# Performance work log

Hardware: AMD Instinct MI355X
Metric: run time of the kernel (lower is better)

The kernel has to match this reference:

```python
import jax, jax.numpy as jnp
import numpy as np

B, L, H = 2, 2048, 1024
NH, DK, DV = 4, 256, 256
CONV_K, FIR_S, FIR_L = 4, 3, 63
GATE_IN = H + 4 * 2 * NH  # 1056
MLP_H = 2 * H
CHUNK = 32


def l2norm(x):
    return x * jax.lax.rsqrt(jnp.sum(x * x, -1, keepdims=True) + 1e-6)


def causal_dwconv(x, w):
    # x: [b, l, c], w: [c, k]; causal depthwise cross-correlation == F.conv1d(pad left k-1, groups=c)
    k = w.shape[-1]
    xc = jnp.pad(jnp.transpose(x, (0, 2, 1)), ((0, 0), (0, 0), (k - 1, 0)))
    y = jax.lax.conv_general_dilated(xc, w[:, None, :], (1,), 'VALID',
                                     feature_group_count=w.shape[0],
                                     dimension_numbers=('NCH', 'OIH', 'NCH'))
    return jnp.transpose(y, (0, 2, 1))


def delta_rule_chunkwise(q, k, v, beta, chunk=CHUNK):
    # q,k: [b,h,L,dk]; v: [b,h,L,dv]; beta: [b,h,L]; L divisible by chunk
    b, h, Lp, dk = q.shape
    dv = v.shape[-1]
    n = Lp // chunk
    q = l2norm(q)
    k = l2norm(k)
    v = v * beta[..., None]
    kb = k * beta[..., None]
    qc, kc, vc, kbc = (t.reshape(b, h, n, chunk, -1) for t in (q, k, v, kb))
    # strictly-lower Gram matrix; the original in-place row loop computes inv(I + tril(kb k^T, -1))
    A = jnp.tril(jnp.einsum('bhnid,bhnjd->bhnij', kbc, kc), -1)
    T = jnp.linalg.inv(jnp.eye(chunk, dtype=q.dtype) + A)  # [b,h,n,c,c]
    u = T @ vc   # [b,h,n,c,dv]
    w = T @ kbc  # [b,h,n,c,dk]

    def step(S, inp):
        qi, ki, ui, wi = inp  # each [b,h,c,d]
        attn = jnp.tril(qi @ jnp.swapaxes(ki, -1, -2))  # keep diag (masked_fill triu(.,1))
        u2 = ui - wi @ S
        oi = qi @ S + attn @ u2
        return S + jnp.swapaxes(ki, -1, -2) @ u2, oi

    S0 = jnp.zeros((b, h, dk, dv), q.dtype)
    xs = tuple(jnp.moveaxis(t, 2, 0) for t in (qc, kc, u, w))
    S, o = jax.lax.scan(step, S0, xs)
    o = jnp.moveaxis(o, 0, 2).reshape(b, h, Lp, dv)
    return o, S


def branch_stats(x):
    # x: [b,l,h,d] -> [b,l,2h]  (mean and population-std, std clamped at sqrt(1e-6))
    m = x.mean(-1)
    s = jnp.sqrt(jnp.maximum(x.var(-1), 1e-6))
    return jnp.concatenate([m, s], -1)


def setup_inputs() -> dict:
    key = jax.random.key(0)
    ks = jax.random.split(key, 16)
    f32 = jnp.float32

    def dirac(k_, shape):
        f = 0.01 * jax.random.normal(k_, shape, f32)
        return f.at[..., shape[-1] // 2].add(1.0)

    b2 = jnp.zeros((NH * 4,), f32).at[jnp.arange(NH) * 4 + 3].set(2.0)
    return {
        'hidden_states': jax.random.normal(ks[0], (B, L, H), f32),
        'Wq': 0.02 * jax.random.normal(ks[1], (H, NH * DK), f32),
        'Wk': 0.02 * jax.random.normal(ks[2], (H, NH * DK), f32),
        'Wv': 0.02 * jax.random.normal(ks[3], (H, NH * DV), f32),
        'Wb': 0.02 * jax.random.normal(ks[4], (H, NH), f32),
        'conv_q_w': 0.2 * jax.random.normal(ks[5], (NH * DK, CONV_K), f32),
        'conv_k_w': 0.2 * jax.random.normal(ks[6], (NH * DK, CONV_K), f32),
        'conv_v_w': 0.2 * jax.random.normal(ks[7], (NH * DV, CONV_K), f32),
        'fir_short_w': dirac(ks[8], (NH, DV, FIR_S)),
        'fir_long_w': dirac(ks[9], (NH, DV, FIR_L)),
        'mlp_w1': 0.02 * jax.random.normal(ks[10], (GATE_IN, MLP_H), f32),
        'mlp_b1': jnp.zeros((MLP_H,), f32),
        'mlp_w2': 0.02 * jax.random.normal(ks[11], (MLP_H, NH * 4), f32),
        'mlp_b2': b2,
        'gate_log_temp': jnp.full((NH,), np.log(1.2), f32),
        'o_norm_w': jnp.ones((DV,), f32),
        'Wo': 0.02 * jax.random.normal(ks[12], (NH * DV, H), f32),
    }


def reference(hidden_states, Wq, Wk, Wv, Wb, conv_q_w, conv_k_w, conv_v_w,
              fir_short_w, fir_long_w, mlp_w1, mlp_b1, mlp_w2, mlp_b2,
              gate_log_temp, o_norm_w, Wo):
    x = hidden_states
    b, l, _ = x.shape
    # projections + short causal depthwise convs with silu (qk_activation='silu')
    q = jax.nn.silu(causal_dwconv(x @ Wq, conv_q_w)).reshape(b, l, NH, DK)
    k = jax.nn.silu(causal_dwconv(x @ Wk, conv_k_w)).reshape(b, l, NH, DK)
    v = jax.nn.silu(causal_dwconv(x @ Wv, conv_v_w)).reshape(b, l, NH, DV)
    beta = jax.nn.sigmoid(x @ Wb)  # [b,l,h]

    delta_out, _S = delta_rule_chunkwise(
        jnp.transpose(q, (0, 2, 1, 3)), jnp.transpose(k, (0, 2, 1, 3)),
        jnp.transpose(v, (0, 2, 1, 3)), jnp.transpose(beta, (0, 2, 1)))
    delta_out = jnp.transpose(delta_out, (0, 2, 1, 3))  # [b,l,h,dv]

    vf = v.reshape(b, l, NH * DV)
    fir_short = causal_dwconv(vf, fir_short_w.reshape(NH * DV, FIR_S)).reshape(b, l, NH, DV)
    fir_long = causal_dwconv(vf, fir_long_w.reshape(NH * DV, FIR_L)).reshape(b, l, NH, DV)

    gate_in = jnp.concatenate([x, branch_stats(fir_short), branch_stats(fir_long),
                               branch_stats(delta_out), branch_stats(v)], -1)
    logits = jax.nn.gelu(gate_in @ mlp_w1 + mlp_b1, approximate=False) @ mlp_w2 + mlp_b2
    temp = jax.nn.softplus(gate_log_temp) + 1e-4
    logits = logits.reshape(b, l, NH, 4) / temp[None, None, :, None]
    w = jax.nn.softmax(logits, -1)

    o = (w[..., 0:1] * fir_short + w[..., 1:2] * fir_long
         + w[..., 2:3] * delta_out + w[..., 3:4] * v)
    # RMSNorm over head_v_dim, eps=1e-5
    o = o * jax.lax.rsqrt(jnp.mean(o * o, -1, keepdims=True) + 1e-5) * o_norm_w
    return o.reshape(b, l, NH * DV) @ Wo
```

## Files before the change

kernel.cpp:

```cpp
#include <hip/hip_runtime.h>
#include <hip/hip_bf16.h>


#define DEVI __device__ __forceinline__
typedef unsigned int u32;
typedef unsigned short ushort_t;
typedef __attribute__((ext_vector_type(8))) short short8;
typedef __attribute__((ext_vector_type(4))) float floatx4;

constexpr int Ls = 2048, NH = 4;
constexpr int NCh = 64;

constexpr size_t off_xq   = 0;
constexpr size_t off_xk   = 4194304;
constexpr size_t off_xv   = 8388608;
constexpr size_t off_q    = 12582912;
constexpr size_t off_k    = 16777216;
constexpr size_t off_v    = 20971520;
constexpr size_t off_beta = 25165824;
constexpr size_t off_attn = 25182208;
constexpr size_t off_firs = 25706496;
constexpr size_t off_firl = 29900800;
constexpr size_t off_gin  = 34095104;
constexpr size_t off_mlph = 38420480;
constexpr size_t off_gates= 46809088;

DEVI float sigmoidf_(float x) { return 1.f / (1.f + expf(-x)); }
DEVI float siluf_(float x) { return x / (1.f + expf(-x)); }
DEVI float geluf_(float x) { return 0.5f * x * (1.f + erff(x * 0.7071067811865476f)); }
DEVI ushort_t f2bf(float f) {
  union { float f; u32 u; } c{f};
  u32 r = (c.u + 0x7fffu + ((c.u >> 16) & 1u)) >> 16;
  return (ushort_t)r;
}
DEVI float bf2f(ushort_t h) {
  union { u32 u; float f; } c; c.u = ((u32)h) << 16; return c.f;
}
DEVI void cvt8(float4 a, float4 b, short8& hi, short8& lo) {
  float f[8] = {a.x,a.y,a.z,a.w,b.x,b.y,b.z,b.w};
#pragma unroll
  for (int j = 0; j < 8; ++j) {
    ushort_t h = f2bf(f[j]);
    hi[j] = (short)h;
    lo[j] = (short)f2bf(f[j] - bf2f(h));
  }
}
DEVI void async16(const void* g, void* l) {
  __builtin_amdgcn_global_load_lds(
      (const u32 __attribute__((address_space(1)))*)g,
      (u32 __attribute__((address_space(3)))*)l, 16, 0, 0);
}

__global__ __launch_bounds__(256) void to_bf16(
    const float* __restrict__ in, ushort_t* __restrict__ out, int n)
{
  int i = (blockIdx.x * 256 + threadIdx.x) * 8;
  if (i >= n) return;
  float4 a = *(const float4*)(in + i);
  float4 b = *(const float4*)(in + i + 4);
  ushort_t o[8] = { f2bf(a.x), f2bf(a.y), f2bf(a.z), f2bf(a.w),
                    f2bf(b.x), f2bf(b.y), f2bf(b.z), f2bf(b.w) };
  *(uint4*)(out + i) = *(uint4*)o;
}

__global__ __launch_bounds__(256) void convT(
    const float* __restrict__ W, ushort_t* __restrict__ out, int Kq, int Nq)
{
  __shared__ ushort_t tile[32][33];
  int n0 = blockIdx.x * 32, k0 = blockIdx.y * 32;
  int tx = threadIdx.x & 31, ty = threadIdx.x >> 5;
#pragma unroll
  for (int r = 0; r < 32; r += 8)
    tile[ty + r][tx] = f2bf(W[(size_t)(k0 + ty + r) * Nq + n0 + tx]);
  __syncthreads();
#pragma unroll
  for (int r = 0; r < 32; r += 8)
    out[(size_t)(n0 + ty + r) * Kq + k0 + tx] = tile[tx][ty + r];
}

__global__ __launch_bounds__(256) void gemm_bf16(
    const ushort_t* __restrict__ A, const ushort_t* __restrict__ Bt,
    float* __restrict__ C, int Nq, int Kq,
    const float* __restrict__ bias, int act, int outbf)
// ... 112 lines not shown
    if (ls >= 0) {
      size_t rb = (size_t)ls * 3072;
      aq = fmaf(qw[j], p[rb], aq);
      ak = fmaf(kw[j], p[rb + 1024], ak);
      av = fmaf(vw[j], p[rb + 2048], av);
    }
  }
  float qv = siluf_(aq), kv = siluf_(ak), vv = siluf_(av);
  float sq = qv * qv, sk = kv * kv;
#pragma unroll
  for (int off = 32; off; off >>= 1) {
    sq += __shfl_down(sq, off);
    sk += __shfl_down(sk, off);
  }
  __shared__ float rq_[4], rk_[4];
  int w = t >> 6;
  if ((t & 63) == 0) { rq_[w] = sq; rk_[w] = sk; }
  __syncthreads();
  sq = rq_[0] + rq_[1] + rq_[2] + rq_[3];
  sk = rk_[0] + rk_[1] + rk_[2] + rk_[3];
  float rq = rsqrtf(sq + 1e-6f), rk = rsqrtf(sk + 1e-6f);
  float bt = beta_g[i];
  size_t base = (size_t)i * 256 + t;
  qn[base] = qv * rq;
  kn[base] = kv * rk;
  kb[base] = kv * rk * bt;
  vb[base] = vv * bt;
  v_out[base] = vv;
}

__global__ __launch_bounds__(256) void chunk_prep(
    const float* __restrict__ kb, const float* __restrict__ kn,
    const float* __restrict__ qn, const float* __restrict__ vb,
    float* __restrict__ attn_g, float* __restrict__ u_out,
    ushort_t* __restrict__ wn_bf, ushort_t* __restrict__ q_bf,
    ushort_t* __restrict__ knT_bf)
{
  __shared__ float Am[32][33];
  __shared__ float Tm[32][36];
  __shared__ ushort_t KT_hi[256][40];
  __shared__ ushort_t KT_lo[256][40];
  int t = threadIdx.x;
  int cc = blockIdx.x & 63, bh = blockIdx.x >> 6;
  size_t gbase = ((size_t)bh * Ls + cc * 32) * 256;
  int wv = t >> 6, lane = t & 63;
  int l16 = lane & 15, quad = lane >> 4;
  int mi = wv >> 1, ni = wv & 1;

  floatx4 Aacc = {0.f,0.f,0.f,0.f}, Qacc = {0.f,0.f,0.f,0.f};
  {
    int mrow = mi * 16 + l16, nrow = ni * 16 + l16;
    const float* kbp = kb + gbase + (size_t)mrow * 256;
    const float* qnp = qn + gbase + (size_t)mrow * 256;
    const float* knp = kn + gbase + (size_t)nrow * 256;
#pragma unroll
    for (int ks = 0; ks < 8; ++ks) {
      int koff = ks * 32 + quad * 8;
      short8 kbh, kbl, qnh, qnl, knh, knl;
      cvt8(*(const float4*)(kbp + koff), *(const float4*)(kbp + koff + 4), kbh, kbl);
      cvt8(*(const float4*)(qnp + koff), *(const float4*)(qnp + koff + 4), qnh, qnl);
      cvt8(*(const float4*)(knp + koff), *(const float4*)(knp + koff + 4), knh, knl);
      Aacc = __builtin_amdgcn_mfma_f32_16x16x32_bf16(kbh, knh, Aacc, 0, 0, 0);
      Aacc = __builtin_amdgcn_mfma_f32_16x16x32_bf16(kbh, knl, Aacc, 0, 0, 0);
      Aacc = __builtin_amdgcn_mfma_f32_16x16x32_bf16(kbl, knh, Aacc, 0, 0, 0);
      Qacc = __builtin_amdgcn_mfma_f32_16x16x32_bf16(qnh, knh, Qacc, 0, 0, 0);
      Qacc = __builtin_amdgcn_mfma_f32_16x16x32_bf16(qnh, knl, Qacc, 0, 0, 0);
      Qacc = __builtin_amdgcn_mfma_f32_16x16x32_bf16(qnl, knh, Qacc, 0, 0, 0);
      if (ni == 0)
        *(uint4*)(q_bf + gbase + (size_t)mrow * 256 + koff) = *(uint4*)&qnh;
    }
  }
  float* ag = attn_g + ((size_t)bh * 64 + cc) * 1024;
#pragma unroll
  for (int r = 0; r < 4; ++r) {
    int row = mi * 16 + quad * 4 + r, col = ni * 16 + l16;
    Am[row][col] = (col < row) ? Aacc[r] : 0.f;
    ag[row * 32 + col] = (col <= row) ? Qacc[r] : 0.f;
  }
  __syncthreads();

  if (wv == 0) {
    if (t < 32) {
#pragma unroll
      for (int i = 0; i < 32; ++i) Tm[i][t] = (i == t) ? 1.f : 0.f;
      for (int i2 = 1; i2 < 32; ++i2) {
        if (t < i2) {
          float s = 0.f;
          for (int m2 = t; m2 < i2; ++m2) s = fmaf(Am[i2][m2], Tm[m2][t], s);
          Tm[i2][t] = -s;
        }
      }
    }
  } else {
    int base = t - 64;
#pragma unroll
    for (int pass = 0; pass < 2; ++pass) {
      int d = base + pass * 192;
      if (d < 256) {
        u32 hp[16], lp[16], kp2[16];
#pragma unroll
        for (int m2 = 0; m2 < 16; ++m2) {
          float f0 = kb[gbase + (size_t)(2 * m2) * 256 + d];
          float f1 = kb[gbase + (size_t)(2 * m2 + 1) * 256 + d];
          ushort_t h0 = f2bf(f0), h1 = f2bf(f1);
          hp[m2] = (u32)h0 | ((u32)h1 << 16);
          lp[m2] = (u32)f2bf(f0 - bf2f(h0)) | ((u32)f2bf(f1 - bf2f(h1)) << 16);
          float g0 = kn[gbase + (size_t)(2 * m2) * 256 + d];
          float g1 = kn[gbase + (size_t)(2 * m2 + 1) * 256 + d];
          kp2[m2] = (u32)f2bf(g0) | ((u32)f2bf(g1) << 16);
        }
#pragma unroll
        for (int q2 = 0; q2 < 4; ++q2) {
          *(uint4*)&KT_hi[d][q2 * 8] = *(uint4*)&hp[q2 * 4];
          *(uint4*)&KT_lo[d][q2 * 8] = *(uint4*)&lp[q2 * 4];
          *(uint4*)(knT_bf + gbase + (size_t)d * 32 + q2 * 8) = *(uint4*)&kp2[q2 * 4];
        }
      }
    }
  }
  __syncthreads();

  int lt = wv & 1, dgrp = wv >> 1;
  short8 Th, Tl;
  {
    int lrow = lt * 16 + l16;
    cvt8(*(const float4*)&Tm[lrow][quad * 8],
         *(const float4*)&Tm[lrow][quad * 8 + 4], Th, Tl);
  }
#pragma unroll
  for (int j = 0; j < 8; ++j) {
    int dt = dgrp * 8 + j;
    short8 Bh = *(const short8*)&KT_hi[dt * 16 + l16][quad * 8];
    short8 Bl = *(const short8*)&KT_lo[dt * 16 + l16][quad * 8];
    floatx4 acc = {0.f,0.f,0.f,0.f};
    acc = __builtin_amdgcn_mfma_f32_16x16x32_bf16(Th, Bh, acc, 0, 0, 0);
    acc = __builtin_amdgcn_mfma_f32_16x16x32_bf16(Th, Bl, acc, 0, 0, 0);
    acc = __builtin_amdgcn_mfma_f32_16x16x32_bf16(Tl, Bh, acc, 0, 0, 0);
#pragma unroll
    for (int r = 0; r < 4; ++r) {
      int row = lt * 16 + quad * 4 + r;
      wn_bf[gbase + (size_t)row * 256 + dt * 16 + l16] = f2bf(-acc[r]);
    }
  }
  __syncthreads();

  {
    int d = t;
    u32 hp[16], lp[16];
#pragma unroll
    for (int m2 = 0; m2 < 16; ++m2) {
      float f0 = vb[gbase + (size_t)(2 * m2) * 256 + d];
      float f1 = vb[gbase + (size_t)(2 * m2 + 1) * 256 + d];
      ushort_t h0 = f2bf(f0), h1 = f2bf(f1);
      hp[m2] = (u32)h0 | ((u32)h1 << 16);
      lp[m2] = (u32)f2bf(f0 - bf2f(h0)) | ((u32)f2bf(f1 - bf2f(h1)) << 16);
    }
#pragma unroll
    for (int q2 = 0; q2 < 4; ++q2) {
      *(uint4*)&KT_hi[d][q2 * 8] = *(uint4*)&hp[q2 * 4];
      *(uint4*)&KT_lo[d][q2 * 8] = *(uint4*)&lp[q2 * 4];
    }
  }
  __syncthreads();

#pragma unroll
  for (int j = 0; j < 8; ++j) {
    int dt = dgrp * 8 + j;
    short8 Bh = *(const short8*)&KT_hi[dt * 16 + l16][quad * 8];
    short8 Bl = *(const short8*)&KT_lo[dt * 16 + l16][quad * 8];
    floatx4 acc = {0.f,0.f,0.f,0.f};
    acc = __builtin_amdgcn_mfma_f32_16x16x32_bf16(Th, Bh, acc, 0, 0, 0);
    acc = __builtin_amdgcn_mfma_f32_16x16x32_bf16(Th, Bl, acc, 0, 0, 0);
    acc = __builtin_amdgcn_mfma_f32_16x16x32_bf16(Tl, Bh, acc, 0, 0, 0);
#pragma unroll
    for (int r = 0; r < 4; ++r) {
      int row = lt * 16 + quad * 4 + r;
      u_out[gbase + (size_t)row * 256 + dt * 16 + l16] = acc[r];
    }
  }
}

__global__ __launch_bounds__(256, 1) void delta_fir(
    const ushort_t* __restrict__ wn_bf, const ushort_t* __restrict__ q_bf,
    const ushort_t* __restrict__ knT_bf, const float* __restrict__ attn_g,
    const float* __restrict__ u_g, float* __restrict__ delta_g,
    const float* __restrict__ v, const float* __restrict__ wlg,
    const float* __restrict__ wsg, float* __restrict__ firl,
    float* __restrict__ firs)
{
  __shared__ __attribute__((aligned(16))) char smem[72704];
  int t = threadIdx.x;

  if (blockIdx.x >= 128) {
    float (*vt)[71] = (float(*)[71])smem;
    int bid = blockIdx.x - 128;
    int lt = bid & 255;
    int bh = bid >> 8;
    int b = bh >> 2, h = bh & 3;
    int l0 = lt * 8;
    const float* vp = v + (size_t)bh * Ls * 256;
    for (int r = 0; r < 70; ++r) {
      int ls = l0 - 62 + r;
      vt[t][r] = (ls >= 0) ? vp[(size_t)ls * 256 + t] : 0.f;
    }
    float TL[63], TS3[3];
#pragma unroll
    for (int j = 0; j < 63; ++j) TL[j] = wlg[((size_t)h * 256 + t) * 63 + j];
#pragma unroll
    for (int j = 0; j < 3; ++j) TS3[j] = wsg[((size_t)h * 256 + t) * 3 + j];
    __syncthreads();
    float aL[8] = {0,0,0,0,0,0,0,0}, aS[8] = {0,0,0,0,0,0,0,0};
#pragma unroll
    for (int r = 0; r < 70; ++r) {
      float vm = vt[t][r];
#pragma unroll
      for (int p = 0; p < 8; ++p) {
        int jl = r - p;
        if (jl >= 0 && jl < 63) aL[p] = fmaf(vm, TL[jl], aL[p]);
        int jssrc = r - 60 - p;
        if (jssrc >= 0 && jssrc < 3) aS[p] = fmaf(vm, TS3[jssrc], aS[p]);
      }
    }
#pragma unroll
    for (int p = 0; p < 8; ++p) {
      int l = l0 + p;
      size_t ob = (((size_t)b * Ls + l) * NH + h) * 256 + t;
      firl[ob] = aL[p];
      firs[ob] = aS[p];
    }
    return;
  }

  ushort_t (*Shi)[264] = (ushort_t(*)[264])(smem);
  ushort_t (*Slo)[264] = (ushort_t(*)[264])(smem + 8448);
  float (*u2L)[17] = (float(*)[17])(smem + 16896);
  int bh = blockIdx.x & 7, g = blockIdx.x >> 3;
  int b = bh >> 2, h = bh & 3;
  int wv = t >> 6, lane = t & 63;
  int lquad = lane >> 4, l16 = lane & 15;
  int j0 = g * 16;
  const ushort_t* wp = wn_bf + (size_t)bh * Ls * 256;
  const ushort_t* qp = q_bf  + (size_t)bh * Ls * 256;
  const ushort_t* kp = knT_bf + (size_t)bh * Ls * 256;
  const float* up = u_g + (size_t)bh * Ls * 256;
  const float* atp = attn_g + (size_t)bh * 64 * 1024;
  int Mt = wv & 1;
  bool isU = (wv < 2);
  floatx4 Sacc[4], SaccL[4];
#pragma unroll
  for (int i = 0; i < 4; ++i)
#pragma unroll
    for (int r = 0; r < 4; ++r) { Sacc[i][r] = 0.f; SaccL[i][r] = 0.f; }
  for (int i = t; i < 4224; i += 256) ((u32*)smem)[i] = 0;
  __syncthreads();
  const ushort_t* ap = (isU ? wp : qp) + (size_t)(Mt * 16 + l16) * 256;
  const ushort_t* kr = kp + (size_t)l16 * 32 + lquad * 8;
  const float* urow = up + (size_t)(Mt * 16 + lquad * 4) * 256 + j0 + l16;
  const float* arp = atp + (size_t)(Mt * 16 + l16) * 32 + lquad * 8;

  short8 aC[8], kC[4];
  floatx4 uC = {0.f, 0.f, 0.f, 0.f};
  float4 atC0 = {0,0,0,0}, atC1 = {0,0,0,0};
#pragma unroll
  for (int ks = 0; ks < 8; ++ks)
    aC[ks] = *(const short8*)(ap + ks * 32 + lquad * 8);
#pragma unroll
  for (int i = 0; i < 4; ++i)
    kC[i] = *(const short8*)(kr + (size_t)(wv * 4 + i) * 512);
  if (isU) {
#pragma unroll
    for (int r = 0; r < 4; ++r) uC[r] = urow[(size_t)r * 256];
  } else {
    atC0 = *(const float4*)(arp);
    atC1 = *(const float4*)(arp + 4);
  }

  for (int cc = 0; cc < NCh; ++cc) {
    size_t cb = (size_t)cc * 8192;
    short8 aN[8], kN[4];
    floatx4 uN = {0.f, 0.f, 0.f, 0.f};
    float4 atN0 = {0,0,0,0}, atN1 = {0,0,0,0};
    bool hasN = (cc + 1 < NCh);
    if (hasN) {
      size_t nb = cb + 8192;
#pragma unroll
      for (int ks = 0; ks < 8; ++ks)
        aN[ks] = *(const short8*)(ap + nb + ks * 32 + lquad * 8);
#pragma unroll
      for (int i = 0; i < 4; ++i)
        kN[i] = *(const short8*)(kr + nb + (size_t)(wv * 4 + i) * 512);
      if (isU) {
#pragma unroll
        for (int r = 0; r < 4; ++r) uN[r] = urow[nb + (size_t)r * 256];
      } else {
        size_t na = (size_t)(cc + 1) * 1024;
        atN0 = *(const float4*)(arp + na);
        atN1 = *(const float4*)(arp + na + 4);
      }
    }
    short8 ath, atl;
    if (!isU) cvt8(atC0, atC1, ath, atl);

    floatx4 acc;
    if (isU) {
      floatx4 a0 = uC, a1 = {0,0,0,0}, a2 = {0,0,0,0}, a3 = {0,0,0,0};
#pragma unroll
      for (int ks = 0; ks < 8; ++ks) {
        short8 sh = *(const short8*)&Shi[l16][ks * 32 + lquad * 8];
        short8 sl = *(const short8*)&Slo[l16][ks * 32 + lquad * 8];
        if (ks & 1) {
          a1 = __builtin_amdgcn_mfma_f32_16x16x32_bf16(aC[ks], sh, a1, 0, 0, 0);
          a3 = __builtin_amdgcn_mfma_f32_16x16x32_bf16(aC[ks], sl, a3, 0, 0, 0);
        } else {
          a0 = __builtin_amdgcn_mfma_f32_16x16x32_bf16(aC[ks], sh, a0, 0, 0, 0);
          a2 = __builtin_amdgcn_mfma_f32_16x16x32_bf16(aC[ks], sl, a2, 0, 0, 0);
        }
      }
#pragma unroll
      for (int r = 0; r < 4; ++r) acc[r] = (a0[r] + a1[r]) + (a2[r] + a3[r]);
#pragma unroll
      for (int r = 0; r < 4; ++r)
        u2L[Mt * 16 + lquad * 4 + r][l16] = acc[r];
    } else {
      floatx4 a0 = {0,0,0,0}, a1 = {0,0,0,0};
#pragma unroll
      for (int ks = 0; ks < 8; ++ks) {
        short8 sh = *(const short8*)&Shi[l16][ks * 32 + lquad * 8];
        if (ks & 1) a1 = __builtin_amdgcn_mfma_f32_16x16x32_bf16(aC[ks], sh, a1, 0, 0, 0);
        else        a0 = __builtin_amdgcn_mfma_f32_16x16x32_bf16(aC[ks], sh, a0, 0, 0, 0);
      }
#pragma unroll
      for (int r = 0; r < 4; ++r) acc[r] = a0[r] + a1[r];
    }
    __syncthreads();
    short8 uh, ul;
#pragma unroll
    for (int j = 0; j < 8; ++j) {
      float f = u2L[lquad * 8 + j][l16];
      ushort_t hi = f2bf(f);
      uh[j] = (short)hi;
      ul[j] = (short)f2bf(f - bf2f(hi));
    }
    if (!isU) {
      acc = __builtin_amdgcn_mfma_f32_16x16x32_bf16(ath, uh, acc, 0, 0, 0);
      acc = __builtin_amdgcn_mfma_f32_16x16x32_bf16(ath, ul, acc, 0, 0, 0);
      acc = __builtin_amdgcn_mfma_f32_16x16x32_bf16(atl, uh, acc, 0, 0, 0);
#pragma unroll
      for (int r = 0; r < 4; ++r) {
        int l = cc * 32 + Mt * 16 + lquad * 4 + r;
        delta_g[(((size_t)b * Ls + l) * NH + h) * 256 + j0 + l16] = acc[r];
      }
    }
#pragma unroll
    for (int i = 0; i < 4; ++i) {
      Sacc[i]  = __builtin_amdgcn_mfma_f32_16x16x32_bf16(kC[i], uh, Sacc[i], 0, 0, 0);
      SaccL[i] = __builtin_amdgcn_mfma_f32_16x16x32_bf16(kC[i], ul, SaccL[i], 0, 0, 0);
    }
#pragma unroll
    for (int i = 0; i < 4; ++i) {
      int dk0 = (wv * 4 + i) * 16 + lquad * 4;
      ushort4 h4, l4;
      ushort_t* hp = (ushort_t*)&h4;
      ushort_t* lp = (ushort_t*)&l4;
#pragma unroll
      for (int r = 0; r < 4; ++r) {
        float sv = Sacc[i][r] + SaccL[i][r];
        ushort_t hi = f2bf(sv);
        hp[r] = hi;
        lp[r] = f2bf(sv - bf2f(hi));
      }
      *(ushort4*)&Shi[l16][dk0] = h4;
      *(ushort4*)&Slo[l16][dk0] = l4;
    }
    __syncthreads();
    if (hasN) {
#pragma unroll
      for (int ks = 0; ks < 8; ++ks) aC[ks] = aN[ks];
#pragma unroll
      for (int i = 0; i < 4; ++i) kC[i] = kN[i];
      uC = uN;
      atC0 = atN0; atC1 = atN1;
    }
  }
}

__global__ __launch_bounds__(256) void build_gate_in_bf(
    const float* __restrict__ x, const float* __restrict__ firs,
    const float* __restrict__ firl, const float* __restrict__ delta,
    const float* __restrict__ v, ushort_t* __restrict__ gin)
{
  int mtok = blockIdx.x, t = threadIdx.x;
  int b = mtok >> 11, l = mtok & 2047;
  float4 xv = *(const float4*)(x + (size_t)mtok * 1024 + t * 4);
  ushort4 xo = make_ushort4(f2bf(xv.x), f2bf(xv.y), f2bf(xv.z), f2bf(xv.w));
  *(ushort4*)(gin + (size_t)mtok * 1056 + t * 4) = xo;
  int w = t >> 6, lane = t & 63;
  for (int br = 0; br < 4; ++br) {
    float s = 0.f, s2 = 0.f;
#pragma unroll
    for (int r = 0; r < 4; ++r) {
      int d = lane + r * 64;
      float val;
      if (br == 0)      val = firs [(size_t)mtok * 1024 + w * 256 + d];
      else if (br == 1) val = firl [(size_t)mtok * 1024 + w * 256 + d];
      else if (br == 2) val = delta[(size_t)mtok * 1024 + w * 256 + d];
      else              val = v[(((size_t)(b * NH + w)) * Ls + l) * 256 + d];
      s += val; s2 = fmaf(val, val, s2);
    }
#pragma unroll
    for (int off = 32; off; off >>= 1) {
      s += __shfl_down(s, off);
      s2 += __shfl_down(s2, off);
    }
    if (lane == 0) {
      float mean = s * (1.f / 256.f);
// ... 83 lines not shown

extern "C" void kernel_launch(void* const* d_in, const int* in_sizes, int n_in,
                              void* d_out, int out_size, void* d_ws, size_t ws_size,
                              hipStream_t stream) {
  const float* x     = (const float*)d_in[0];
  const float* Wq    = (const float*)d_in[1];
  const float* Wk    = (const float*)d_in[2];
  const float* Wv    = (const float*)d_in[3];
  const float* Wb    = (const float*)d_in[4];
  const float* convq = (const float*)d_in[5];
  const float* convk = (const float*)d_in[6];
  const float* convv = (const float*)d_in[7];
  const float* firsw = (const float*)d_in[8];
  const float* firlw = (const float*)d_in[9];
  const float* mlpw1 = (const float*)d_in[10];
  const float* mlpb1 = (const float*)d_in[11];
  const float* mlpw2 = (const float*)d_in[12];
  const float* mlpb2 = (const float*)d_in[13];
  const float* glt   = (const float*)d_in[14];
  const float* onw   = (const float*)d_in[15];
  const float* Wo    = (const float*)d_in[16];
  float* ws = (float*)d_ws;

  ushort_t* x_bf   = (ushort_t*)(ws + off_firs);
  ushort_t* Wqkv_t = (ushort_t*)(ws + off_firl);
  ushort_t* gin_bf = (ushort_t*)(ws + off_gin);
  ushort_t* w1_t   = (ushort_t*)(ws + off_k);
  ushort_t* o_bf   = (ushort_t*)(ws + off_xv);
  ushort_t* Wo_t   = (ushort_t*)(ws + off_beta);
  ushort_t* mlph_bf= (ushort_t*)(ws + off_mlph);
  ushort_t* wn_bf  = (ushort_t*)(ws + off_firs);
  ushort_t* q_bf   = (ushort_t*)(ws + off_firs + 2097152);
  ushort_t* knT_bf = (ushort_t*)(ws + off_firl);
  float* x3   = ws + off_xq;
  float* kb_f = ws + off_gin;
  float* vb_f = ws + off_mlph;
  float* firs_f = ws + off_xq;
  float* firl_f = ws + off_xk;

  dim3 blk(256);
  to_bf16<<<2048, blk, 0, stream>>>(x, x_bf, 4194304);
  convT<<<dim3(32, 32), blk, 0, stream>>>(Wq, Wqkv_t, 1024, 1024);
  convT<<<dim3(32, 32), blk, 0, stream>>>(Wk, Wqkv_t + 1048576, 1024, 1024);
  convT<<<dim3(32, 32), blk, 0, stream>>>(Wv, Wqkv_t + 2097152, 1024, 1024);
  gemm_bf16<<<dim3(24, 32), blk, 0, stream>>>(x_bf, Wqkv_t, x3, 3072, 1024, nullptr, 0, 0);
  beta_sigmoid<<<4096, blk, 0, stream>>>(x, Wb, ws + off_beta);
  conv_prep<<<16384, blk, 0, stream>>>(x3, convq, convk, convv, ws + off_beta,
                                       ws + off_q, ws + off_k, kb_f, vb_f, ws + off_v);
  chunk_prep<<<512, blk, 0, stream>>>(kb_f, ws + off_k, ws + off_q, vb_f,
                                      ws + off_attn, ws + off_xv, wn_bf, q_bf, knT_bf);
  delta_fir<<<2176, blk, 0, stream>>>(wn_bf, q_bf, knT_bf, ws + off_attn,
                                      ws + off_xv, ws + off_q,
                                      ws + off_v, firlw, firsw, firl_f, firs_f);
  build_gate_in_bf<<<4096, blk, 0, stream>>>(x, firs_f, firl_f, ws + off_q,
                                             ws + off_v, gin_bf);
  convT<<<dim3(64, 33), blk, 0, stream>>>(mlpw1, w1_t, 1056, 2048);
  gemm_bf16<<<dim3(16, 32), blk, 0, stream>>>(gin_bf, w1_t, (float*)mlph_bf,
                                              2048, 1056, mlpb1, 1, 1);
  mlp2_gates<<<4096, blk, 0, stream>>>(mlph_bf, mlpw2, mlpb2, glt, ws + off_gates);
  combine_norm_bf<<<16384, blk, 0, stream>>>(firs_f, firl_f, ws + off_q,
                                             ws + off_v, ws + off_gates, onw, o_bf);
  convT<<<dim3(32, 32), blk, 0, stream>>>(Wo, Wo_t, 1024, 1024);
  gemm_bf16<<<dim3(8, 32), blk, 0, stream>>>(o_bf, Wo_t, (float*)d_out, 1024, 1024, nullptr, 0, 0);
}
```

Before: 581.9 us.

## Merge 32-token chunks into 128-token groups for the delta-rule recurrence

Adds a group_prep kernel that merges four 32-token chunks into one 128-token group. It builds the block-triangular inverse from the per-chunk T matrices and cross-chunk Gram products, corrects w and u, and forms a 128x128 causal q·k attention matrix stored as bf16 hi/lo pairs. The sequential delta_fir loop then runs 16 group steps instead of 64 chunk steps, cutting the serial state-update and barrier count by four. In exchange it adds a kernel launch and extra workspace traffic, the cross-chunk attention terms lose precision (single bf16 product, low part of q and k dropped), and the per-step register footprint and work grow.

```diff
diff --git a/kernel.cpp b/kernel.cpp
--- a/kernel.cpp
+++ b/kernel.cpp
@@ -9,7 +9,6 @@
 typedef __attribute__((ext_vector_type(4))) float floatx4;
 
 constexpr int Ls = 2048, NH = 4;
-constexpr int NCh = 64;
 
 constexpr size_t off_xq   = 0;
 constexpr size_t off_xk   = 4194304;
@@ -23,6 +22,7 @@
 constexpr size_t off_firl = 29900800;
 constexpr size_t off_gin  = 34095104;
 constexpr size_t off_mlph = 38420480;
+constexpr size_t off_at   = 42614784;
 constexpr size_t off_gates= 46809088;
 
 DEVI float sigmoidf_(float x) { return 1.f / (1.f + expf(-x)); }
@@ -49,6 +49,12 @@
   __builtin_amdgcn_global_load_lds(
       (const u32 __attribute__((address_space(1)))*)g,
       (u32 __attribute__((address_space(3)))*)l, 16, 0, 0);
+}
+DEVI void wave_barrier() {
+  __builtin_amdgcn_sched_barrier(0);
+  asm volatile("s_waitcnt lgkmcnt(0)" ::: "memory");
+  __builtin_amdgcn_s_barrier();
+  __builtin_amdgcn_sched_barrier(0);
 }
 
 __global__ __launch_bounds__(256) void to_bf16(
@@ -227,9 +233,10 @@
 __global__ __launch_bounds__(256) void chunk_prep(
     const float* __restrict__ kb, const float* __restrict__ kn,
     const float* __restrict__ qn, const float* __restrict__ vb,
-    float* __restrict__ attn_g, float* __restrict__ u_out,
+    float* __restrict__ u_out,
     ushort_t* __restrict__ wn_bf, ushort_t* __restrict__ q_bf,
-    ushort_t* __restrict__ knT_bf)
+    ushort_t* __restrict__ knT_bf, ushort_t* __restrict__ kn_bf,
+    float* __restrict__ T_g)
 {
   __shared__ float Am[32][33];
   __shared__ float Tm[32][36];
@@ -242,7 +249,7 @@
   int l16 = lane & 15, quad = lane >> 4;
   int mi = wv >> 1, ni = wv & 1;
 
-  floatx4 Aacc = {0.f,0.f,0.f,0.f}, Qacc = {0.f,0.f,0.f,0.f};
+  floatx4 Aacc = {0.f,0.f,0.f,0.f};
   {
     int mrow = mi * 16 + l16, nrow = ni * 16 + l16;
     const float* kbp = kb + gbase + (size_t)mrow * 256;
@@ -258,19 +265,16 @@
       Aacc = __builtin_amdgcn_mfma_f32_16x16x32_bf16(kbh, knh, Aacc, 0, 0, 0);
       Aacc = __builtin_amdgcn_mfma_f32_16x16x32_bf16(kbh, knl, Aacc, 0, 0, 0);
       Aacc = __builtin_amdgcn_mfma_f32_16x16x32_bf16(kbl, knh, Aacc, 0, 0, 0);
-      Qacc = __builtin_amdgcn_mfma_f32_16x16x32_bf16(qnh, knh, Qacc, 0, 0, 0);
-      Qacc = __builtin_amdgcn_mfma_f32_16x16x32_bf16(qnh, knl, Qacc, 0, 0, 0);
-      Qacc = __builtin_amdgcn_mfma_f32_16x16x32_bf16(qnl, knh, Qacc, 0, 0, 0);
       if (ni == 0)
         *(uint4*)(q_bf + gbase + (size_t)mrow * 256 + koff) = *(uint4*)&qnh;
-    }
-  }
-  float* ag = attn_g + ((size_t)bh * 64 + cc) * 1024;
+      if (mi == 0)
+        *(uint4*)(kn_bf + gbase + (size_t)nrow * 256 + koff) = *(uint4*)&knh;
+    }
+  }
 #pragma unroll
   for (int r = 0; r < 4; ++r) {
     int row = mi * 16 + quad * 4 + r, col = ni * 16 + l16;
     Am[row][col] = (col < row) ? Aacc[r] : 0.f;
-    ag[row * 32 + col] = (col <= row) ? Qacc[r] : 0.f;
   }
   __syncthreads();
 
@@ -315,6 +319,9 @@
   }
   __syncthreads();
 
+  *(float4*)(T_g + ((size_t)(bh * 64 + cc)) * 1024 + t * 4) =
+      *(const float4*)&Tm[t >> 3][(t & 7) * 4];
+
   int lt = wv & 1, dgrp = wv >> 1;
   short8 Th, Tl;
   {
@@ -375,10 +382,248 @@
   }
 }
 
+DEVI void rowfrag_hl(const float (*M)[36], int row, int q4, short8& h, short8& l) {
+  const float* p = &M[row][q4 * 8];
+#pragma unroll
+  for (int jj = 0; jj < 8; ++jj) {
+    ushort_t hi = f2bf(p[jj]);
+    h[jj] = (short)hi;
+    l[jj] = (short)f2bf(p[jj] - bf2f(hi));
+  }
+}
+DEVI void colfrag_hl(const float* M, int q4, int col, short8& h, short8& l) {
+#pragma unroll
+  for (int jj = 0; jj < 8; ++jj) {
+    float f = M[(size_t)(q4 * 8 + jj) * 256 + col];
+    ushort_t hi = f2bf(f);
+    h[jj] = (short)hi;
+    l[jj] = (short)f2bf(f - bf2f(hi));
+  }
+}
+DEVI void mm32(const float (*A)[36], const float (*B)[36],
+               floatx4 acc[2][2], int l16, int q4, bool negA)
+{
+#pragma unroll
+  for (int mt = 0; mt < 2; ++mt) {
+    float4 a0 = *(const float4*)&A[mt * 16 + l16][q4 * 8];
+    float4 a1 = *(const float4*)&A[mt * 16 + l16][q4 * 8 + 4];
+    if (negA) {
+      a0.x = -a0.x; a0.y = -a0.y; a0.z = -a0.z; a0.w = -a0.w;
+      a1.x = -a1.x; a1.y = -a1.y; a1.z = -a1.z; a1.w = -a1.w;
+    }
+    short8 Ah, Al; cvt8(a0, a1, Ah, Al);
+#pragma unroll
+    for (int nt = 0; nt < 2; ++nt) {
+      float4 b0, b1;
+      b0.x = B[q4*8+0][nt*16+l16]; b0.y = B[q4*8+1][nt*16+l16];
+      b0.z = B[q4*8+2][nt*16+l16]; b0.w = B[q4*8+3][nt*16+l16];
+      b1.x = B[q4*8+4][nt*16+l16]; b1.y = B[q4*8+5][nt*16+l16];
+      b1.z = B[q4*8+6][nt*16+l16]; b1.w = B[q4*8+7][nt*16+l16];
+      short8 Bh, Bl; cvt8(b0, b1, Bh, Bl);
+      acc[mt][nt] = __builtin_amdgcn_mfma_f32_16x16x32_bf16(Ah, Bh, acc[mt][nt], 0, 0, 0);
+      acc[mt][nt] = __builtin_amdgcn_mfma_f32_16x16x32_bf16(Ah, Bl, acc[mt][nt], 0, 0, 0);
+      acc[mt][nt] = __builtin_amdgcn_mfma_f32_16x16x32_bf16(Al, Bh, acc[mt][nt], 0, 0, 0);
+    }
+  }
+}
+DEVI void st32(float (*O)[36], floatx4 acc[2][2], int l16, int q4)
+{
+#pragma unroll
+  for (int mt = 0; mt < 2; ++mt)
+#pragma unroll
+    for (int nt = 0; nt < 2; ++nt)
+#pragma unroll
+      for (int r = 0; r < 4; ++r)
+        O[mt * 16 + q4 * 4 + r][nt * 16 + l16] = acc[mt][nt][r];
+}
+
+__global__ __launch_bounds__(256) void group_prep(
+    const float* __restrict__ T_g, const float* __restrict__ kb,
+    const float* __restrict__ vb, const float* __restrict__ qn,
+    const float* __restrict__ knf, const ushort_t* __restrict__ kn_bf,
+    const ushort_t* __restrict__ q_bf, ushort_t* __restrict__ wn_bf,
+    float* __restrict__ u_g, ushort_t* __restrict__ at_hi,
+    ushort_t* __restrict__ at_lo)
+{
+  __shared__ float Ts[4][32][36];
+  __shared__ float Gs[6][32][36];
+  __shared__ float Bs[6][32][36];
+  int t = threadIdx.x;
+  int grp = blockIdx.x & 15, bh = blockIdx.x >> 4;
+  int wv = t >> 6, lane = t & 63;
+  int l16 = lane & 15, q4 = lane >> 4;
+  size_t base = ((size_t)bh * Ls + grp * 128) * 256;
+  size_t abase = ((size_t)bh * 16 + grp) * 16384;
+  floatx4 z4 = {0.f, 0.f, 0.f, 0.f};
+
+  {
+    const float* tp = T_g + ((size_t)(bh * 64 + grp * 4 + wv)) * 1024;
+    for (int e = lane; e < 1024; e += 64)
+      Ts[wv][e >> 5][e & 31] = tp[e];
+  }
+  for (int e = t; e < 6144; e += 256) {
+    int blk = e >> 10, idx = e & 1023;
+    int bi = blk < 3 ? 0 : (blk < 5 ? 1 : 2);
+    int bj = blk < 3 ? blk + 1 : (blk < 5 ? blk - 1 : 3);
+    size_t off = abase + (size_t)(bi * 32 + (idx >> 5)) * 128 + bj * 32 + (idx & 31);
+    at_hi[off] = 0; at_lo[off] = 0;
+  }
+  __syncthreads();
+
+  {
+    int mt = wv >> 1, nt = wv & 1;
+#pragma unroll
+    for (int pid = 0; pid < 6; ++pid) {
+      int gi = (pid < 1) ? 1 : (pid < 3 ? 2 : 3);
+      int gj = pid - gi * (gi - 1) / 2;
+      const float* ap = kb + base + (size_t)(gi * 32 + mt * 16 + l16) * 256;
+      const float* bp = knf + base + (size_t)(gj * 32 + nt * 16 + l16) * 256;
+      floatx4 acc = z4;
+#pragma unroll
+      for (int ks = 0; ks < 8; ++ks) {
+        int ko = ks * 32 + q4 * 8;
+        short8 ah, al, bbh, bbl;
+        cvt8(*(const float4*)(ap + ko), *(const float4*)(ap + ko + 4), ah, al);
+        cvt8(*(const float4*)(bp + ko), *(const float4*)(bp + ko + 4), bbh, bbl);
+        acc = __builtin_amdgcn_mfma_f32_16x16x32_bf16(ah, bbh, acc, 0, 0, 0);
+        acc = __builtin_amdgcn_mfma_f32_16x16x32_bf16(ah, bbl, acc, 0, 0, 0);
+        acc = __builtin_amdgcn_mfma_f32_16x16x32_bf16(al, bbh, acc, 0, 0, 0);
+      }
+#pragma unroll
+      for (int r = 0; r < 4; ++r)
+        Gs[pid][mt * 16 + q4 * 4 + r][nt * 16 + l16] = acc[r];
+    }
+#pragma unroll
+    for (int c = 0; c < 4; ++c) {
+      const float* ap = qn + base + (size_t)(c * 32 + mt * 16 + l16) * 256;
+      const float* bp = knf + base + (size_t)(c * 32 + nt * 16 + l16) * 256;
+      floatx4 acc = z4;
+#pragma unroll
+      for (int ks = 0; ks < 8; ++ks) {
+        int ko = ks * 32 + q4 * 8;
+        short8 ah, al, bbh, bbl;
+        cvt8(*(const float4*)(ap + ko), *(const float4*)(ap + ko + 4), ah, al);
+        cvt8(*(const float4*)(bp + ko), *(const float4*)(bp + ko + 4), bbh, bbl);
+        acc = __builtin_amdgcn_mfma_f32_16x16x32_bf16(ah, bbh, acc, 0, 0, 0);
+        acc = __builtin_amdgcn_mfma_f32_16x16x32_bf16(ah, bbl, acc, 0, 0, 0);
+        acc = __builtin_amdgcn_mfma_f32_16x16x32_bf16(al, bbh, acc, 0, 0, 0);
+      }
+#pragma unroll
+      for (int r = 0; r < 4; ++r) {
+        int row = mt * 16 + q4 * 4 + r, col = nt * 16 + l16;
+        float vv2 = (col <= row) ? acc[r] : 0.f;
+        ushort_t hi = f2bf(vv2);
+        size_t off = abase + (size_t)(c * 32 + row) * 128 + c * 32 + col;
+        at_hi[off] = hi;
+        at_lo[off] = f2bf(vv2 - bf2f(hi));
+      }
+    }
+  }
+  __syncthreads();
+
+  if (wv < 3) {
+    int ii = wv + 1, jj = wv;
+    int pid = ii * (ii - 1) / 2 + jj;
+    floatx4 acc[2][2] = {{z4, z4}, {z4, z4}};
+    mm32(Gs[pid], Ts[jj], acc, l16, q4, false);
+    st32(Bs[pid], acc, l16, q4);
+    floatx4 acc2[2][2] = {{z4, z4}, {z4, z4}};
+    mm32(Ts[ii], Bs[pid], acc2, l16, q4, true);
+    st32(Bs[pid], acc2, l16, q4);
+  }
+  __syncthreads();
+  if (wv < 2) {
+    int ii = wv + 2, jj = wv;
+    int pid  = ii * (ii - 1) / 2 + jj;
+    int pidA = ii * (ii - 1) / 2 + jj + 1;
+    int pidB = (jj + 1) * jj / 2 + jj;
+    floatx4 acc[2][2] = {{z4, z4}, {z4, z4}};
+    mm32(Gs[pid],  Ts[jj],   acc, l16, q4, false);
+    mm32(Gs[pidA], Bs[pidB], acc, l16, q4, false);
+    st32(Bs[pid], acc, l16, q4);
+    floatx4 acc2[2][2] = {{z4, z4}, {z4, z4}};
+    mm32(Ts[ii], Bs[pid], acc2, l16, q4, true);
+    st32(Bs[pid], acc2, l16, q4);
+  }
+  __syncthreads();
+  if (wv == 0) {
+    floatx4 acc[2][2] = {{z4, z4}, {z4, z4}};
+    mm32(Gs[3], Ts[0], acc, l16, q4, false);
+    mm32(Gs[4], Bs[0], acc, l16, q4, false);
+    mm32(Gs[5], Bs[1], acc, l16, q4, false);
+    st32(Bs[3], acc, l16, q4);
+    floatx4 acc2[2][2] = {{z4, z4}, {z4, z4}};
+    mm32(Ts[3], Bs[3], acc2, l16, q4, true);
+    st32(Bs[3], acc2, l16, q4);
+  }
+  __syncthreads();
+
+#pragma unroll
+  for (int i = 1; i < 4; ++i) {
+#pragma unroll
+    for (int Rt = 0; Rt < 2; ++Rt) {
+      short8 Ah[3], Al[3];
+#pragma unroll
+      for (int j = 0; j < 3; ++j)
+        if (j < i) rowfrag_hl(Bs[i * (i - 1) / 2 + j], Rt * 16 + l16, q4, Ah[j], Al[j]);
+#pragma unroll
+      for (int dt = 0; dt < 4; ++dt) {
+        int dcol = (wv * 4 + dt) * 16 + l16;
+        floatx4 accW = z4, accU = z4;
+#pragma unroll
+        for (int j = 0; j < 3; ++j) {
+          if (j < i) {
+            short8 Bwh, Bwl, Buh, Bul;
+            colfrag_hl(kb + base + (size_t)j * 8192, q4, dcol, Bwh, Bwl);
+            colfrag_hl(vb + base + (size_t)j * 8192, q4, dcol, Buh, Bul);
+            accW = __builtin_amdgcn_mfma_f32_16x16x32_bf16(Ah[j], Bwh, accW, 0, 0, 0);
+            accW = __builtin_amdgcn_mfma_f32_16x16x32_bf16(Ah[j], Bwl, accW, 0, 0, 0);
+            accW = __builtin_amdgcn_mfma_f32_16x16x32_bf16(Al[j], Bwh, accW, 0, 0, 0);
+            accU = __builtin_amdgcn_mfma_f32_16x16x32_bf16(Ah[j], Buh, accU, 0, 0, 0);
+            accU = __builtin_amdgcn_mfma_f32_16x16x32_bf16(Ah[j], Bul, accU, 0, 0, 0);
+            accU = __builtin_amdgcn_mfma_f32_16x16x32_bf16(Al[j], Buh, accU, 0, 0, 0);
+          }
+        }
+#pragma unroll
+        for (int r = 0; r < 4; ++r) {
+          size_t off = base + (size_t)(i * 32 + Rt * 16 + q4 * 4 + r) * 256 + dcol;
+          wn_bf[off] = f2bf(bf2f(wn_bf[off]) - accW[r]);
+          u_g[off] += accU[r];
+        }
+      }
+    }
+  }
+
+  for (int tt = wv; tt < 24; tt += 4) {
+    int pid = tt >> 2, mt = (tt >> 1) & 1, nt = tt & 1;
+    int gi = (pid < 1) ? 1 : (pid < 3 ? 2 : 3);
+    int gj = pid - gi * (gi - 1) / 2;
+    const ushort_t* ap = q_bf + base + (size_t)(gi * 32 + mt * 16 + l16) * 256;
+    const ushort_t* bp = kn_bf + base + (size_t)(gj * 32 + nt * 16 + l16) * 256;
+    floatx4 acc = z4;
+#pragma unroll
+    for (int ks = 0; ks < 8; ++ks) {
+      short8 aq = *(const short8*)(ap + ks * 32 + q4 * 8);
+      short8 bk = *(const short8*)(bp + ks * 32 + q4 * 8);
+      acc = __builtin_amdgcn_mfma_f32_16x16x32_bf16(aq, bk, acc, 0, 0, 0);
+    }
+#pragma unroll
+    for (int r = 0; r < 4; ++r) {
+      float vv2 = acc[r];
+      ushort_t hi = f2bf(vv2);
+      size_t off = abase + (size_t)(gi * 32 + mt * 16 + q4 * 4 + r) * 128
+                 + gj * 32 + nt * 16 + l16;
+      at_hi[off] = hi;
+      at_lo[off] = f2bf(vv2 - bf2f(hi));
+    }
+  }
+}
+
 __global__ __launch_bounds__(256, 1) void delta_fir(
     const ushort_t* __restrict__ wn_bf, const ushort_t* __restrict__ q_bf,
-    const ushort_t* __restrict__ knT_bf, const float* __restrict__ attn_g,
-    const float* __restrict__ u_g, float* __restrict__ delta_g,
+    const ushort_t* __restrict__ knT_bf, const ushort_t* __restrict__ at_hi,
+    const ushort_t* __restrict__ at_lo, const float* __restrict__ u_g,
+    float* __restrict__ delta_g,
     const float* __restrict__ v, const float* __restrict__ wlg,
     const float* __restrict__ wsg, float* __restrict__ firl,
     float* __restrict__ firs)
@@ -428,132 +673,138 @@
 
   ushort_t (*Shi)[264] = (ushort_t(*)[264])(smem);
   ushort_t (*Slo)[264] = (ushort_t(*)[264])(smem + 8448);
-  float (*u2L)[17] = (float(*)[17])(smem + 16896);
+  float (*u2L)[18] = (float(*)[18])(smem + 16896);
   int bh = blockIdx.x & 7, g = blockIdx.x >> 3;
   int b = bh >> 2, h = bh & 3;
   int wv = t >> 6, lane = t & 63;
-  int lquad = lane >> 4, l16 = lane & 15;
+  int q4 = lane >> 4, l16 = lane & 15;
   int j0 = g * 16;
-  const ushort_t* wp = wn_bf + (size_t)bh * Ls * 256;
-  const ushort_t* qp = q_bf  + (size_t)bh * Ls * 256;
-  const ushort_t* kp = knT_bf + (size_t)bh * Ls * 256;
-  const float* up = u_g + (size_t)bh * Ls * 256;
-  const float* atp = attn_g + (size_t)bh * 64 * 1024;
-  int Mt = wv & 1;
   bool isU = (wv < 2);
+  int rb = (isU ? wv : (wv - 2)) * 64;
+  const ushort_t* ap_ = (isU ? wn_bf : q_bf) + (size_t)bh * Ls * 256;
+  const ushort_t* krb = knT_bf + (size_t)bh * Ls * 256;
+  const float* ub = u_g + (size_t)bh * Ls * 256;
+  const ushort_t* ahb = at_hi + (size_t)bh * 16 * 16384;
+  const ushort_t* alb = at_lo + (size_t)bh * 16 * 16384;
+
   floatx4 Sacc[4], SaccL[4];
 #pragma unroll
   for (int i = 0; i < 4; ++i)
 #pragma unroll
     for (int r = 0; r < 4; ++r) { Sacc[i][r] = 0.f; SaccL[i][r] = 0.f; }
   for (int i = t; i < 4224; i += 256) ((u32*)smem)[i] = 0;
-  __syncthreads();
-  const ushort_t* ap = (isU ? wp : qp) + (size_t)(Mt * 16 + l16) * 256;
-  const ushort_t* kr = kp + (size_t)l16 * 32 + lquad * 8;
-  const float* urow = up + (size_t)(Mt * 16 + lquad * 4) * 256 + j0 + l16;
-  const float* arp = atp + (size_t)(Mt * 16 + l16) * 32 + lquad * 8;
-
-  short8 aC[8], kC[4];
-  floatx4 uC = {0.f, 0.f, 0.f, 0.f};
-  float4 atC0 = {0,0,0,0}, atC1 = {0,0,0,0};
-#pragma unroll
-  for (int ks = 0; ks < 8; ++ks)
-    aC[ks] = *(const short8*)(ap + ks * 32 + lquad * 8);
-#pragma unroll
-  for (int i = 0; i < 4; ++i)
-    kC[i] = *(const short8*)(kr + (size_t)(wv * 4 + i) * 512);
-  if (isU) {
-#pragma unroll
-    for (int r = 0; r < 4; ++r) uC[r] = urow[(size_t)r * 256];
-  } else {
-    atC0 = *(const float4*)(arp);
-    atC1 = *(const float4*)(arp + 4);
-  }
-
-  for (int cc = 0; cc < NCh; ++cc) {
-    size_t cb = (size_t)cc * 8192;
-    short8 aN[8], kN[4];
-    floatx4 uN = {0.f, 0.f, 0.f, 0.f};
-    float4 atN0 = {0,0,0,0}, atN1 = {0,0,0,0};
-    bool hasN = (cc + 1 < NCh);
-    if (hasN) {
-      size_t nb = cb + 8192;
-#pragma unroll
-      for (int ks = 0; ks < 8; ++ks)
-        aN[ks] = *(const short8*)(ap + nb + ks * 32 + lquad * 8);
+  wave_barrier();
+
+  for (int grp = 0; grp < 16; ++grp) {
+    size_t gb = (size_t)grp * 32768;
+    size_t ab = (size_t)grp * 16384;
+    short8 kf[4][4];
+#pragma unroll
+    for (int kt = 0; kt < 4; ++kt)
 #pragma unroll
       for (int i = 0; i < 4; ++i)
-        kN[i] = *(const short8*)(kr + nb + (size_t)(wv * 4 + i) * 512);
+        kf[kt][i] = *(const short8*)(krb + gb + (size_t)kt * 8192
+                     + (size_t)((wv * 4 + i) * 16 + l16) * 32 + q4 * 8);
+    floatx4 uin[4];
+    floatx4 po[4];
+    if (isU) {
+#pragma unroll
+      for (int mt = 0; mt < 4; ++mt)
+#pragma unroll
+        for (int r = 0; r < 4; ++r)
+          uin[mt][r] = ub[gb + (size_t)(rb + mt * 16 + q4 * 4 + r) * 256 + j0 + l16];
+    }
+    short8 frA[8], frB[8];
+#pragma unroll
+    for (int ks = 0; ks < 8; ++ks)
+      frA[ks] = *(const short8*)(ap_ + gb + (size_t)(rb + l16) * 256 + ks * 32 + q4 * 8);
+#pragma unroll
+    for (int mt = 0; mt < 4; ++mt) {
+      if (mt < 3) {
+#pragma unroll
+        for (int ks = 0; ks < 8; ++ks) {
+          short8 ld = *(const short8*)(ap_ + gb
+                       + (size_t)(rb + (mt + 1) * 16 + l16) * 256 + ks * 32 + q4 * 8);
+          if (mt & 1) frA[ks] = ld; else frB[ks] = ld;
+        }
+      }
       if (isU) {
-#pragma unroll
-        for (int r = 0; r < 4; ++r) uN[r] = urow[nb + (size_t)r * 256];
+        floatx4 A0 = uin[mt], A1 = {0,0,0,0}, A2 = {0,0,0,0}, A3 = {0,0,0,0};
+#pragma unroll
+        for (int ks = 0; ks < 8; ++ks) {
+          short8 aw = (mt & 1) ? frB[ks] : frA[ks];
+          short8 sh = *(const short8*)&Shi[l16][ks * 32 + q4 * 8];
+          short8 sl = *(const short8*)&Slo[l16][ks * 32 + q4 * 8];
+          if (ks & 1) {
+            A1 = __builtin_amdgcn_mfma_f32_16x16x32_bf16(aw, sh, A1, 0, 0, 0);
+            A3 = __builtin_amdgcn_mfma_f32_16x16x32_bf16(aw, sl, A3, 0, 0, 0);
+          } else {
+            A0 = __builtin_amdgcn_mfma_f32_16x16x32_bf16(aw, sh, A0, 0, 0, 0);
+            A2 = __builtin_amdgcn_mfma_f32_16x16x32_bf16(aw, sl, A2, 0, 0, 0);
+          }
+        }
+#pragma unroll
+        for (int r = 0; r < 4; ++r)
+          u2L[rb + mt * 16 + q4 * 4 + r][l16] = (A0[r] + A1[r]) + (A2[r] + A3[r]);
       } else {
-        size_t na = (size_t)(cc + 1) * 1024;
-        atN0 = *(const float4*)(arp + na);
-        atN1 = *(const float4*)(arp + na + 4);
-      }
-    }
-    short8 ath, atl;
-    if (!isU) cvt8(atC0, atC1, ath, atl);
-
-    floatx4 acc;
-    if (isU) {
-      floatx4 a0 = uC, a1 = {0,0,0,0}, a2 = {0,0,0,0}, a3 = {0,0,0,0};
-#pragma unroll
-      for (int ks = 0; ks < 8; ++ks) {
-        short8 sh = *(const short8*)&Shi[l16][ks * 32 + lquad * 8];
-        short8 sl = *(const short8*)&Slo[l16][ks * 32 + lquad * 8];
-        if (ks & 1) {
-          a1 = __builtin_amdgcn_mfma_f32_16x16x32_bf16(aC[ks], sh, a1, 0, 0, 0);
-          a3 = __builtin_amdgcn_mfma_f32_16x16x32_bf16(aC[ks], sl, a3, 0, 0, 0);
-        } else {
-          a0 = __builtin_amdgcn_mfma_f32_16x16x32_bf16(aC[ks], sh, a0, 0, 0, 0);
-          a2 = __builtin_amdgcn_mfma_f32_16x16x32_bf16(aC[ks], sl, a2, 0, 0, 0);
+        floatx4 A0 = {0,0,0,0}, A1 = {0,0,0,0};
+#pragma unroll
+        for (int ks = 0; ks < 8; ++ks) {
+          short8 aw = (mt & 1) ? frB[ks] : frA[ks];
+          short8 sh = *(const short8*)&Shi[l16][ks * 32 + q4 * 8];
+          if (ks & 1) A1 = __builtin_amdgcn_mfma_f32_16x16x32_bf16(aw, sh, A1, 0, 0, 0);
+          else        A0 = __builtin_amdgcn_mfma_f32_16x16x32_bf16(aw, sh, A0, 0, 0, 0);
         }
-      }
-#pragma unroll
-      for (int r = 0; r < 4; ++r) acc[r] = (a0[r] + a1[r]) + (a2[r] + a3[r]);
-#pragma unroll
-      for (int r = 0; r < 4; ++r)
-        u2L[Mt * 16 + lquad * 4 + r][l16] = acc[r];
-    } else {
-      floatx4 a0 = {0,0,0,0}, a1 = {0,0,0,0};
-#pragma unroll
-      for (int ks = 0; ks < 8; ++ks) {
-        short8 sh = *(const short8*)&Shi[l16][ks * 32 + lquad * 8];
-        if (ks & 1) a1 = __builtin_amdgcn_mfma_f32_16x16x32_bf16(aC[ks], sh, a1, 0, 0, 0);
-        else        a0 = __builtin_amdgcn_mfma_f32_16x16x32_bf16(aC[ks], sh, a0, 0, 0, 0);
-      }
-#pragma unroll
-      for (int r = 0; r < 4; ++r) acc[r] = a0[r] + a1[r];
-    }
-    __syncthreads();
-    short8 uh, ul;
-#pragma unroll
-    for (int j = 0; j < 8; ++j) {
-      float f = u2L[lquad * 8 + j][l16];
-      ushort_t hi = f2bf(f);
-      uh[j] = (short)hi;
-      ul[j] = (short)f2bf(f - bf2f(hi));
+#pragma unroll
+        for (int r = 0; r < 4; ++r) po[mt][r] = A0[r] + A1[r];
+      }
+    }
+    wave_barrier();
+
+#pragma unroll
+    for (int kt = 0; kt < 4; ++kt) {
+      short8 uh, ul;
+      {
+        float4 a_, b_;
+        a_.x = u2L[kt * 32 + q4 * 8 + 0][l16];
+        a_.y = u2L[kt * 32 + q4 * 8 + 1][l16];
+        a_.z = u2L[kt * 32 + q4 * 8 + 2][l16];
+        a_.w = u2L[kt * 32 + q4 * 8 + 3][l16];
+        b_.x = u2L[kt * 32 + q4 * 8 + 4][l16];
+        b_.y = u2L[kt * 32 + q4 * 8 + 5][l16];
+        b_.z = u2L[kt * 32 + q4 * 8 + 6][l16];
+        b_.w = u2L[kt * 32 + q4 * 8 + 7][l16];
+        cvt8(a_, b_, uh, ul);
+      }
+#pragma unroll
+      for (int i = 0; i < 4; ++i) {
+        Sacc[i]  = __builtin_amdgcn_mfma_f32_16x16x32_bf16(kf[kt][i], uh, Sacc[i], 0, 0, 0);
+        SaccL[i] = __builtin_amdgcn_mfma_f32_16x16x32_bf16(kf[kt][i], ul, SaccL[i], 0, 0, 0);
+      }
+      if (!isU) {
+#pragma unroll
+        for (int mt = 0; mt < 4; ++mt) {
+          size_t ao = ab + (size_t)(rb + mt * 16 + l16) * 128 + kt * 32 + q4 * 8;
+          short8 ath = *(const short8*)(ahb + ao);
+          short8 atl = *(const short8*)(alb + ao);
+          po[mt] = __builtin_amdgcn_mfma_f32_16x16x32_bf16(ath, uh, po[mt], 0, 0, 0);
+          po[mt] = __builtin_amdgcn_mfma_f32_16x16x32_bf16(ath, ul, po[mt], 0, 0, 0);
+          po[mt] = __builtin_amdgcn_mfma_f32_16x16x32_bf16(atl, uh, po[mt], 0, 0, 0);
+        }
+      }
     }
     if (!isU) {
-      acc = __builtin_amdgcn_mfma_f32_16x16x32_bf16(ath, uh, acc, 0, 0, 0);
-      acc = __builtin_amdgcn_mfma_f32_16x16x32_bf16(ath, ul, acc, 0, 0, 0);
-      acc = __builtin_amdgcn_mfma_f32_16x16x32_bf16(atl, uh, acc, 0, 0, 0);
-#pragma unroll
-      for (int r = 0; r < 4; ++r) {
-        int l = cc * 32 + Mt * 16 + lquad * 4 + r;
-        delta_g[(((size_t)b * Ls + l) * NH + h) * 256 + j0 + l16] = acc[r];
-      }
+#pragma unroll
+      for (int mt = 0; mt < 4; ++mt)
+#pragma unroll
+        for (int r = 0; r < 4; ++r) {
+          int l = grp * 128 + rb + mt * 16 + q4 * 4 + r;
+          delta_g[(((size_t)b * Ls + l) * NH + h) * 256 + j0 + l16] = po[mt][r];
+        }
     }
 #pragma unroll
     for (int i = 0; i < 4; ++i) {
-      Sacc[i]  = __builtin_amdgcn_mfma_f32_16x16x32_bf16(kC[i], uh, Sacc[i], 0, 0, 0);
-      SaccL[i] = __builtin_amdgcn_mfma_f32_16x16x32_bf16(kC[i], ul, SaccL[i], 0, 0, 0);
-    }
-#pragma unroll
-    for (int i = 0; i < 4; ++i) {
-      int dk0 = (wv * 4 + i) * 16 + lquad * 4;
+      int dk0 = (wv * 4 + i) * 16 + q4 * 4;
       ushort4 h4, l4;
       ushort_t* hp = (ushort_t*)&h4;
       ushort_t* lp = (ushort_t*)&l4;
@@ -567,15 +818,7 @@
       *(ushort4*)&Shi[l16][dk0] = h4;
       *(ushort4*)&Slo[l16][dk0] = l4;
     }
-    __syncthreads();
-    if (hasN) {
-#pragma unroll
-      for (int ks = 0; ks < 8; ++ks) aC[ks] = aN[ks];
-#pragma unroll
-      for (int i = 0; i < 4; ++i) kC[i] = kN[i];
-      uC = uN;
-      atC0 = atN0; atC1 = atN1;
-    }
+    wave_barrier();
   }
 }
 
@@ -725,9 +968,13 @@
   ushort_t* wn_bf  = (ushort_t*)(ws + off_firs);
   ushort_t* q_bf   = (ushort_t*)(ws + off_firs + 2097152);
   ushort_t* knT_bf = (ushort_t*)(ws + off_firl);
+  ushort_t* kn_bf  = (ushort_t*)(ws + off_xq);
   float* x3   = ws + off_xq;
   float* kb_f = ws + off_gin;
   float* vb_f = ws + off_mlph;
+  float* T_g  = ws + off_attn;
+  ushort_t* at_hi = (ushort_t*)(ws + off_at);
+  ushort_t* at_lo = (ushort_t*)(ws + off_at + 1048576);
   float* firs_f = ws + off_xq;
   float* firl_f = ws + off_xk;
 
@@ -741,8 +988,11 @@
   conv_prep<<<16384, blk, 0, stream>>>(x3, convq, convk, convv, ws + off_beta,
                                        ws + off_q, ws + off_k, kb_f, vb_f, ws + off_v);
   chunk_prep<<<512, blk, 0, stream>>>(kb_f, ws + off_k, ws + off_q, vb_f,
-                                      ws + off_attn, ws + off_xv, wn_bf, q_bf, knT_bf);
-  delta_fir<<<2176, blk, 0, stream>>>(wn_bf, q_bf, knT_bf, ws + off_attn,
+                                      ws + off_xv, wn_bf, q_bf, knT_bf, kn_bf, T_g);
+  group_prep<<<128, blk, 0, stream>>>(T_g, kb_f, vb_f, ws + off_q, ws + off_k,
+                                      kn_bf, q_bf, wn_bf, ws + off_xv,
+                                      at_hi, at_lo);
+  delta_fir<<<2176, blk, 0, stream>>>(wn_bf, q_bf, knT_bf, at_hi, at_lo,
                                       ws + off_xv, ws + off_q,
                                       ws + off_v, firlw, firsw, firl_f, firs_f);
   build_gate_in_bf<<<4096, blk, 0, stream>>>(x, firs_f, firl_f, ws + off_q,
```

Result: slower. 733.0 us (+26.0%).
